# Optimization experiments

Measured on AMD Instinct MI355X. Metric: run time of the kernel, lower is better.

The kernel has to match this reference:

```python
import jax
import jax.numpy as jnp
from jax import lax
import numpy as np

V, E, H, H2, C, B, L = 50000, 256, 256, 128, 12, 64, 512
START, STOP = 10, 11
IMPOSSIBLE = -10000.0


def setup_inputs() -> dict:
    key = jax.random.key(0)
    ks = jax.random.split(key, 30)
    rn = lambda k, s, sc=0.1: jax.random.normal(k, s, jnp.float32) * sc
    d = {}
    d["sentence"] = jax.random.randint(ks[0], (B, L), 0, V)
    d["masks"] = jnp.ones((B, L), jnp.float32)
    d["emb_table"] = rn(ks[1], (V, E))
    i = 2
    for layer, din in ((1, E), (2, H)):
        for dr in ("f", "r"):
            d["w_ih_%s%d" % (dr, layer)] = rn(ks[i], (4 * H2, din)); i += 1
            d["w_hh_%s%d" % (dr, layer)] = rn(ks[i], (4 * H2, H2)); i += 1
            d["b_ih_%s%d" % (dr, layer)] = rn(ks[i], (4 * H2,)); i += 1
            d["b_hh_%s%d" % (dr, layer)] = rn(ks[i], (4 * H2,)); i += 1
    d["w_out"] = rn(ks[i], (C, H)); i += 1
    d["b_out"] = rn(ks[i], (C,)); i += 1
    tr = jax.random.normal(ks[i], (C, C), jnp.float32); i += 1
    d["transitions"] = tr.at[START, :].set(IMPOSSIBLE).at[:, STOP].set(IMPOSSIBLE)
    for nm in ("h0_1", "c0_1", "h0_2", "c0_2"):
        d[nm] = rn(ks[i], (2, B, H2), 1.0); i += 1
    return d


def _lstm_dir(x, h0, c0, w_ih, w_hh, b_ih, b_hh, reverse):
    # x: [L, B, Din]; PyTorch LSTM gate order: i, f, g, o
    b = b_ih + b_hh
    def step(carry, xt):
        h, c = carry
        g = xt @ w_ih.T + h @ w_hh.T + b  # [B, 4*H2]
        i, f, gg, o = jnp.split(g, 4, axis=-1)
        c = jax.nn.sigmoid(f) * c + jax.nn.sigmoid(i) * jnp.tanh(gg)
        h = jax.nn.sigmoid(o) * jnp.tanh(c)
        return (h, c), h
    _, hs = lax.scan(step, (h0, c0), x, reverse=reverse)
    return hs  # [L, B, H2]


def _bilstm(x, h0, c0, pf, pr):
    hf = _lstm_dir(x, h0[0], c0[0], *pf, reverse=False)
    hr = _lstm_dir(x, h0[1], c0[1], *pr, reverse=True)
    return jnp.concatenate([hf, hr], axis=-1)  # [L, B, H]


def reference(sentence, masks, emb_table,
              w_ih_f1, w_hh_f1, b_ih_f1, b_hh_f1, w_ih_r1, w_hh_r1, b_ih_r1, b_hh_r1,
              w_ih_f2, w_hh_f2, b_ih_f2, b_hh_f2, w_ih_r2, w_hh_r2, b_ih_r2, b_hh_r2,
              w_out, b_out, transitions, h0_1, c0_1, h0_2, c0_2):
    Bb, Ll = sentence.shape
    # faithful to the original: embedding output is .view()'d (reshaped), not transposed
    embeds = emb_table[sentence].reshape(Ll, Bb, -1)  # [L, B, E]
    out1 = _bilstm(embeds, h0_1, c0_1,
                   (w_ih_f1, w_hh_f1, b_ih_f1, b_hh_f1),
                   (w_ih_r1, w_hh_r1, b_ih_r1, b_hh_r1))
    out2 = _bilstm(out1, h0_2, c0_2,
                   (w_ih_f2, w_hh_f2, b_ih_f2, b_hh_f2),
                   (w_ih_r2, w_hh_r2, b_ih_r2, b_hh_r2))
    feats = out2.reshape(Bb, Ll, -1) @ w_out.T + b_out  # [B, L, C]
    Cc = feats.shape[-1]

    # Viterbi forward pass over time
    init = jnp.full((Bb, Cc), IMPOSSIBLE, jnp.float32).at[:, START].set(0.0)
    def vstep(ms, inp):
        emit, m = inp  # [B, C], [B]
        acc = ms[:, None, :] + transitions[None]  # [B, C_to, C_from]
        bp = jnp.argmax(acc, axis=-1)             # [B, C]
        sc = jnp.max(acc, axis=-1) + emit
        mm = m[:, None]
        return sc * mm + ms * (1.0 - mm), bp
    final, bps = lax.scan(vstep, init, (feats.transpose(1, 0, 2), masks.T))  # bps: [L, B, C]
    final = final + transitions[STOP]
    best_score = final.max(axis=-1)        # [B]
    best_tag = jnp.argmax(final, axis=-1)  # [B]

    # vectorized backtrace: tag[len-1] = best_tag; tag[t] = bps[t+1][tag[t+1]]
    lengths = masks.sum(axis=1).astype(jnp.int32)  # [B]
    bps_next = jnp.concatenate([bps[1:], bps[-1:]], axis=0)  # bps_next[t] = bps[t+1]
    ts = jnp.arange(Ll)
    def bstep(cur, inp):
        t, bpn = inp  # bpn: [B, C]
        nxt = jnp.take_along_axis(bpn, cur[:, None], axis=1)[:, 0]
        new = jnp.where(t >= lengths - 1, best_tag, nxt)
        return new, new
    _, path = lax.scan(bstep, best_tag, (ts, bps_next), reverse=True)  # [L, B]
    path = path.T  # [B, L]
    path = jnp.where(ts[None, :] < lengths[:, None], path, 0)
    return best_score, path
```

## Files before the change

kernel.cpp:

```cpp
#include <hip/hip_runtime.h>
#include <math.h>

#define VSZ   50000
#define EDIM  256
#define HDIM  256
#define H2D   128
#define NCLS  12
#define NB    64
#define NL    512
#define G4    512
#define NNC   1024
#define MM    32768
#define START_TAG 10
#define STOP_TAG  11
#define IMPOSSIBLE -10000.0f

__device__ __forceinline__ float sigmoidf_(float x) {
    return 1.0f / (1.0f + expf(-x));
}

template <bool GATHER>
__global__ __launch_bounds__(256)
void gemm_gates(const float* __restrict__ A,
                const int*   __restrict__ gidx,
                const float* __restrict__ wf,
                const float* __restrict__ wr,
                const float* __restrict__ bihf, const float* __restrict__ bhhf,
                const float* __restrict__ bihr, const float* __restrict__ bhhr,
                float* __restrict__ out)
{
    __shared__ __align__(16) float As[32][132];
    __shared__ __align__(16) float Bs[32][132];

    const int tid = threadIdx.x;
    const int n0  = blockIdx.x * 128;
    const int m0  = blockIdx.y * 128;

    const int w    = tid >> 6;
    const int lane = tid & 63;
    const int wm   = w >> 1;
    const int wn   = w & 1;
    const int am   = lane >> 3;
    const int bn   = lane & 7;
    const int ma   = wm * 64 + am * 8;
    const int nb   = wn * 64 + bn * 8;

    float acc[8][8];
#pragma unroll
    for (int i = 0; i < 8; ++i)
#pragma unroll
        for (int jj = 0; jj < 8; ++jj) acc[i][jj] = 0.0f;

    const bool   fwdside = (n0 < 512);
    const float* wsrc    = fwdside ? wf : wr;
    const int    nbase   = fwdside ? n0 : (n0 - 512);

    int srcA[4];
#pragma unroll
    for (int it = 0; it < 4; ++it) {
        int li  = tid + it * 256;
        int row = m0 + (li >> 3);
        srcA[it] = GATHER ? gidx[row] : row;
    }

    for (int kt = 0; kt < 8; ++kt) {
#pragma unroll
        for (int it = 0; it < 4; ++it) {
            int li = tid + it * 256;
            int r  = li >> 3;
            int c4 = li & 7;
            float4 v = ((const float4*)A)[(size_t)srcA[it] * 64 + kt * 8 + c4];
            As[c4 * 4 + 0][r] = v.x;
            As[c4 * 4 + 1][r] = v.y;
            As[c4 * 4 + 2][r] = v.z;
            As[c4 * 4 + 3][r] = v.w;
        }
#pragma unroll
        for (int it = 0; it < 4; ++it) {
            int li = tid + it * 256;
            int r  = li >> 3;
            int c4 = li & 7;
            float4 v = ((const float4*)wsrc)[(size_t)(nbase + r) * 64 + kt * 8 + c4];
            Bs[c4 * 4 + 0][r] = v.x;
            Bs[c4 * 4 + 1][r] = v.y;
            Bs[c4 * 4 + 2][r] = v.z;
            Bs[c4 * 4 + 3][r] = v.w;
        }
        __syncthreads();

#pragma unroll
        for (int k = 0; k < 32; ++k) {
            float a[8], b[8];
            *(float4*)&a[0] = *(const float4*)&As[k][ma];
            *(float4*)&a[4] = *(const float4*)&As[k][ma + 4];
            *(float4*)&b[0] = *(const float4*)&Bs[k][nb];
            *(float4*)&b[4] = *(const float4*)&Bs[k][nb + 4];
#pragma unroll
            for (int i = 0; i < 8; ++i)
#pragma unroll
                for (int jj = 0; jj < 8; ++jj)
                    acc[i][jj] = fmaf(a[i], b[jj], acc[i][jj]);
        }
        __syncthreads();
    }

    float bias[8];
#pragma unroll
    for (int jj = 0; jj < 8; ++jj) {
        int gn = n0 + nb + jj;
        bias[jj] = fwdside ? (bihf[gn] + bhhf[gn]) : (bihr[gn - 512] + bhhr[gn - 512]);
    }
#pragma unroll
    for (int i = 0; i < 8; ++i) {
        int m = m0 + ma + i;
        float4 s0, s1;
        s0.x = acc[i][0] + bias[0]; s0.y = acc[i][1] + bias[1];
        s0.z = acc[i][2] + bias[2]; s0.w = acc[i][3] + bias[3];
        s1.x = acc[i][4] + bias[4]; s1.y = acc[i][5] + bias[5];
        s1.z = acc[i][6] + bias[6]; s1.w = acc[i][7] + bias[7];
        float4* op = (float4*)(out + (size_t)m * NNC + n0 + nb);
        op[0] = s0;
        op[1] = s1;
    }
}

__global__ __launch_bounds__(512, 2)
void lstm_rec(const float* __restrict__ gx,
              const float* __restrict__ whf,
              const float* __restrict__ whr,
              const float* __restrict__ h0,
              const float* __restrict__ c0,
              float* __restrict__ out)
{
    __shared__ __align__(16) float h_lds[H2D];
    __shared__ __align__(16) float gates[G4];

    const int j   = threadIdx.x;
    const int dir = blockIdx.x >> 6;
    const int bb  = blockIdx.x & 63;
    const float* W = dir ? whr : whf;

    float4 w4[32];
#pragma unroll
    for (int k = 0; k < 32; ++k)
        w4[k] = ((const float4*)W)[(size_t)j * 32 + k];
#pragma unroll
    for (int k = 0; k < 32; ++k)
        asm volatile("" : "+v"(w4[k].x), "+v"(w4[k].y), "+v"(w4[k].z), "+v"(w4[k].w));

    float creg = 0.0f;
    if (j < H2D) {
        h_lds[j] = h0[dir * (NB * H2D) + bb * H2D + j];
        creg     = c0[dir * (NB * H2D) + bb * H2D + j];
    }
    __syncthreads();

    const float4* h4 = (const float4*)h_lds;
    const int chunk = j >> 7;
    const size_t gx_off = (size_t)dir * 512 + j;

    const int tfirst = dir ? (NL - 1) : 0;
    float gx_cur = gx[((size_t)tfirst * NB + bb) * NNC + gx_off];

    for (int ti = 0; ti < NL; ++ti) {
        const int t = dir ? (NL - 1 - ti) : ti;
        const size_t m = (size_t)t * NB + bb;

        float d0 = 0.f, d1 = 0.f, d2 = 0.f, d3 = 0.f;
#pragma unroll
        for (int k = 0; k < 32; ++k) {
            const float4 hv = h4[k];
            d0 = fmaf(w4[k].x, hv.x, d0);
            d1 = fmaf(w4[k].y, hv.y, d1);
            d2 = fmaf(w4[k].z, hv.z, d2);
            d3 = fmaf(w4[k].w, hv.w, d3);
        }
        const float pre = ((d0 + d1) + (d2 + d3)) + gx_cur;
        const float act = (chunk == 2) ? tanhf(pre) : sigmoidf_(pre);
        gates[j] = act;
        __syncthreads();

        if (ti + 1 < NL) {
            const int tn = dir ? (NL - 2 - ti) : (ti + 1);
            gx_cur = gx[((size_t)tn * NB + bb) * NNC + gx_off];
        }

        if (j < H2D) {
            const float ig = gates[j];
            const float fg = gates[j + 128];
            const float gg = gates[j + 256];
            const float og = gates[j + 384];
            creg = fg * creg + ig * gg;
            const float hnew = og * tanhf(creg);
            h_lds[j] = hnew;
            out[m * HDIM + dir * H2D + j] = hnew;
        }
        __syncthreads();
    }
}

__global__ __launch_bounds__(256)
void feats_kernel(const float* __restrict__ out2,
                  const float* __restrict__ w_out,
                  const float* __restrict__ b_out,
                  float* __restrict__ feats)
{
    __shared__ __align__(16) float wl[NCLS * HDIM];
    const int tid = threadIdx.x;
#pragma unroll
    for (int i = 0; i < NCLS; ++i) wl[tid + i * 256] = w_out[tid + i * 256];
    __syncthreads();

    const int m = blockIdx.x * 256 + tid;
    float acc[NCLS];
#pragma unroll
    for (int c = 0; c < NCLS; ++c) acc[c] = 0.0f;

    const float4* x4 = (const float4*)out2 + (size_t)m * 64;
    const float4* w4 = (const float4*)wl;
    for (int k4 = 0; k4 < 64; ++k4) {
        float4 x = x4[k4];
#pragma unroll
        for (int c = 0; c < NCLS; ++c) {
            float4 wv = w4[c * 64 + k4];
            acc[c] = fmaf(x.x, wv.x, acc[c]);
            acc[c] = fmaf(x.y, wv.y, acc[c]);
            acc[c] = fmaf(x.z, wv.z, acc[c]);
            acc[c] = fmaf(x.w, wv.w, acc[c]);
        }
    }
#pragma unroll
    for (int c = 0; c < NCLS; ++c)
        feats[(size_t)m * NCLS + c] = acc[c] + b_out[c];
}

__global__ __launch_bounds__(64)
void viterbi_crf(const float* __restrict__ feats,
                 const float* __restrict__ masks,
                 const float* __restrict__ trans,
                 float* __restrict__ out)
{
    __shared__ unsigned char bpl[NL][NCLS];
    __shared__ float pathl[NL];

    const int b    = blockIdx.x;
    const int lane = threadIdx.x;

    float tr[NCLS];
#pragma unroll
    for (int jj = 0; jj < NCLS; ++jj)
        tr[jj] = (lane < NCLS) ? trans[lane * NCLS + jj] : 0.0f;

    float msv = (lane == START_TAG) ? 0.0f : IMPOSSIBLE;
    float len = 0.0f;

    float emit_n = (lane < NCLS) ? feats[((size_t)b * NL) * NCLS + lane] : 0.0f;
    float mt_n   = masks[b * NL];

    for (int t = 0; t < NL; ++t) {
        const float emit = emit_n;
        const float mt   = mt_n;
        if (t + 1 < NL) {
            emit_n = (lane < NCLS) ? feats[((size_t)b * NL + t + 1) * NCLS + lane] : 0.0f;
            mt_n   = masks[b * NL + t + 1];
        }
        len += mt;

        float best = -3.4e38f;
        int   bj   = 0;
#pragma unroll
        for (int jj = 0; jj < NCLS; ++jj) {
            float msj = __shfl(msv, jj);
            float v   = msj + tr[jj];
            if (v > best) { best = v; bj = jj; }
        }
        const float sc = best + emit;
        msv = mt * sc + (1.0f - mt) * msv;
        if (lane < NCLS)
            bpl[t][lane] = (unsigned char)bj;
    }

    const float fin = (lane < NCLS) ? (msv + trans[STOP_TAG * NCLS + lane]) : -3.4e38f;
    float bv = -3.4e38f;
    int   bt = 0;
#pragma unroll
    for (int jj = 0; jj < NCLS; ++jj) {
        float v = __shfl(fin, jj);
        if (v > bv) { bv = v; bt = jj; }
    }
    if (lane == 0) out[b] = bv;

    const int ilen = (int)(len + 0.5f);

    __syncthreads();

    int cur = bt;
    for (int t = NL - 1; t >= 0; --t) {
        const int tb  = (t == NL - 1) ? (NL - 1) : (t + 1);
        const int nxt = bpl[tb][cur];
        const int val = (t >= ilen - 1) ? bt : nxt;
        cur = val;
        if (lane == 0) pathl[t] = (t < ilen) ? (float)val : 0.0f;
    }
    __syncthreads();

    float* po = out + 64 + (size_t)b * NL;
#pragma unroll
    for (int i = 0; i < NL / 64; ++i)
        po[lane + i * 64] = pathl[lane + i * 64];
}

extern "C" void kernel_launch(void* const* d_in, const int* in_sizes, int n_in,
                              void* d_out, int out_size, void* d_ws, size_t ws_size,
                              hipStream_t stream)
{
    const int*   sentence = (const int*)  d_in[0];
    const float* masks    = (const float*)d_in[1];
    const float* emb      = (const float*)d_in[2];
    const float* w_ih_f1  = (const float*)d_in[3];
    const float* w_hh_f1  = (const float*)d_in[4];
    const float* b_ih_f1  = (const float*)d_in[5];
    const float* b_hh_f1  = (const float*)d_in[6];
    const float* w_ih_r1  = (const float*)d_in[7];
    const float* w_hh_r1  = (const float*)d_in[8];
    const float* b_ih_r1  = (const float*)d_in[9];
    const float* b_hh_r1  = (const float*)d_in[10];
    const float* w_ih_f2  = (const float*)d_in[11];
    const float* w_hh_f2  = (const float*)d_in[12];
    const float* b_ih_f2  = (const float*)d_in[13];
    const float* b_hh_f2  = (const float*)d_in[14];
    const float* w_ih_r2  = (const float*)d_in[15];
    const float* w_hh_r2  = (const float*)d_in[16];
    const float* b_ih_r2  = (const float*)d_in[17];
    const float* b_hh_r2  = (const float*)d_in[18];
    const float* w_out    = (const float*)d_in[19];
    const float* b_out    = (const float*)d_in[20];
    const float* trans    = (const float*)d_in[21];
    const float* h0_1     = (const float*)d_in[22];
    const float* c0_1     = (const float*)d_in[23];
    const float* h0_2     = (const float*)d_in[24];
    const float* c0_2     = (const float*)d_in[25];

    float* gx    = (float*)d_ws;
    float* out1  = gx   + (size_t)MM * NNC;
    float* out2  = out1 + (size_t)MM * HDIM;
    float* feats = out2 + (size_t)MM * HDIM;

    dim3 gemm_grid(NNC / 128, MM / 128);

    gemm_gates<true><<<gemm_grid, 256, 0, stream>>>(
        emb, sentence, w_ih_f1, w_ih_r1, b_ih_f1, b_hh_f1, b_ih_r1, b_hh_r1, gx);
    lstm_rec<<<128, 512, 0, stream>>>(gx, w_hh_f1, w_hh_r1, h0_1, c0_1, out1);

    gemm_gates<false><<<gemm_grid, 256, 0, stream>>>(
        out1, nullptr, w_ih_f2, w_ih_r2, b_ih_f2, b_hh_f2, b_ih_r2, b_hh_r2, gx);
    lstm_rec<<<128, 512, 0, stream>>>(gx, w_hh_f2, w_hh_r2, h0_2, c0_2, out2);

    feats_kernel<<<MM / 256, 256, 0, stream>>>(out2, w_out, b_out, feats);
    viterbi_crf<<<NB, 64, 0, stream>>>(feats, masks, trans, (float*)d_out);
}
```

Baseline: 1.872 ms.

## Split LSTM recurrence K-dimension across 1024 threads with readlane broadcast

The recurrent kernel now launches 1024 threads per block, and each thread holds half a weight row (64 values) in registers. The hidden state is broadcast within each wavefront via readlane instead of LDS float4 reads. Partial dot products are summed through shared memory, and the 128 update threads apply all four gate activations and prefetch their own gx values. The goal is to shorten the serial per-timestep latency, at the cost of more threads, more scalar readlane work and higher register pressure per step.

```diff
diff --git a/kernel.cpp b/kernel.cpp
--- a/kernel.cpp
+++ b/kernel.cpp
@@ -124,7 +124,7 @@
     }
 }
 
-__global__ __launch_bounds__(512, 2)
+__global__ __launch_bounds__(1024, 4)
 void lstm_rec(const float* __restrict__ gx,
               const float* __restrict__ whf,
               const float* __restrict__ whr,
@@ -133,67 +133,91 @@
               float* __restrict__ out)
 {
     __shared__ __align__(16) float h_lds[H2D];
-    __shared__ __align__(16) float gates[G4];
-
-    const int j   = threadIdx.x;
+    __shared__ __align__(16) float partial[1024];
+
+    const int tid = threadIdx.x;
+    const int row = tid & 511;
+    const int kh  = tid >> 9;
     const int dir = blockIdx.x >> 6;
     const int bb  = blockIdx.x & 63;
     const float* W = dir ? whr : whf;
 
-    float4 w4[32];
-#pragma unroll
-    for (int k = 0; k < 32; ++k)
-        w4[k] = ((const float4*)W)[(size_t)j * 32 + k];
-#pragma unroll
-    for (int k = 0; k < 32; ++k)
-        asm volatile("" : "+v"(w4[k].x), "+v"(w4[k].y), "+v"(w4[k].z), "+v"(w4[k].w));
+    float wreg[64];
+    {
+        const float4* wp = (const float4*)(W + (size_t)row * H2D + kh * 64);
+#pragma unroll
+        for (int k = 0; k < 16; ++k) {
+            float4 v = wp[k];
+            wreg[4 * k + 0] = v.x; wreg[4 * k + 1] = v.y;
+            wreg[4 * k + 2] = v.z; wreg[4 * k + 3] = v.w;
+        }
+    }
 
     float creg = 0.0f;
-    if (j < H2D) {
-        h_lds[j] = h0[dir * (NB * H2D) + bb * H2D + j];
-        creg     = c0[dir * (NB * H2D) + bb * H2D + j];
+    if (tid < H2D) {
+        h_lds[tid] = h0[dir * (NB * H2D) + bb * H2D + tid];
+        creg       = c0[dir * (NB * H2D) + bb * H2D + tid];
     }
     __syncthreads();
 
-    const float4* h4 = (const float4*)h_lds;
-    const int chunk = j >> 7;
-    const size_t gx_off = (size_t)dir * 512 + j;
-
-    const int tfirst = dir ? (NL - 1) : 0;
-    float gx_cur = gx[((size_t)tfirst * NB + bb) * NNC + gx_off];
+    const int  lane = tid & 63;
+    const bool upd  = (tid < H2D);
+
+    const size_t gxbase = (size_t)dir * 512 + tid;
+    float gxc[4] = {0.f, 0.f, 0.f, 0.f};
+    if (upd) {
+        const int tf = dir ? (NL - 1) : 0;
+        const size_t mo = ((size_t)tf * NB + bb) * NNC + gxbase;
+#pragma unroll
+        for (int k = 0; k < 4; ++k) gxc[k] = gx[mo + 128 * k];
+    }
 
     for (int ti = 0; ti < NL; ++ti) {
         const int t = dir ? (NL - 1 - ti) : ti;
         const size_t m = (size_t)t * NB + bb;
 
-        float d0 = 0.f, d1 = 0.f, d2 = 0.f, d3 = 0.f;
-#pragma unroll
-        for (int k = 0; k < 32; ++k) {
-            const float4 hv = h4[k];
-            d0 = fmaf(w4[k].x, hv.x, d0);
-            d1 = fmaf(w4[k].y, hv.y, d1);
-            d2 = fmaf(w4[k].z, hv.z, d2);
-            d3 = fmaf(w4[k].w, hv.w, d3);
-        }
-        const float pre = ((d0 + d1) + (d2 + d3)) + gx_cur;
-        const float act = (chunk == 2) ? tanhf(pre) : sigmoidf_(pre);
-        gates[j] = act;
+        const float hv  = h_lds[kh * 64 + lane];
+        const int   hvi = __float_as_int(hv);
+
+        float gxn[4];
+        if (upd && ti + 1 < NL) {
+            const int tn = dir ? (NL - 2 - ti) : (ti + 1);
+            const size_t mo = ((size_t)tn * NB + bb) * NNC + gxbase;
+#pragma unroll
+            for (int k = 0; k < 4; ++k) gxn[k] = gx[mo + 128 * k];
+        }
+
+        float a0 = 0.f, a1 = 0.f, a2 = 0.f, a3 = 0.f;
+#pragma unroll
+        for (int i = 0; i < 64; i += 4) {
+            const float s0 = __int_as_float(__builtin_amdgcn_readlane(hvi, i + 0));
+            const float s1 = __int_as_float(__builtin_amdgcn_readlane(hvi, i + 1));
+            const float s2 = __int_as_float(__builtin_amdgcn_readlane(hvi, i + 2));
+            const float s3 = __int_as_float(__builtin_amdgcn_readlane(hvi, i + 3));
+            a0 = fmaf(wreg[i + 0], s0, a0);
+            a1 = fmaf(wreg[i + 1], s1, a1);
+            a2 = fmaf(wreg[i + 2], s2, a2);
+            a3 = fmaf(wreg[i + 3], s3, a3);
+        }
+        const float half = (a0 + a1) + (a2 + a3);
+        partial[tid] = half;
         __syncthreads();
 
-        if (ti + 1 < NL) {
-            const int tn = dir ? (NL - 2 - ti) : (ti + 1);
-            gx_cur = gx[((size_t)tn * NB + bb) * NNC + gx_off];
-        }
-
-        if (j < H2D) {
-            const float ig = gates[j];
-            const float fg = gates[j + 128];
-            const float gg = gates[j + 256];
-            const float og = gates[j + 384];
+        if (upd) {
+            const float pi = (half + partial[tid + 512]) + gxc[0];
+            const float pf = (partial[tid + 128] + partial[tid + 640]) + gxc[1];
+            const float pg = (partial[tid + 256] + partial[tid + 768]) + gxc[2];
+            const float po = (partial[tid + 384] + partial[tid + 896]) + gxc[3];
+            const float ig = sigmoidf_(pi);
+            const float fg = sigmoidf_(pf);
+            const float gg = tanhf(pg);
+            const float og = sigmoidf_(po);
             creg = fg * creg + ig * gg;
             const float hnew = og * tanhf(creg);
-            h_lds[j] = hnew;
-            out[m * HDIM + dir * H2D + j] = hnew;
+            h_lds[tid] = hnew;
+            out[m * HDIM + dir * H2D + tid] = hnew;
+#pragma unroll
+            for (int k = 0; k < 4; ++k) gxc[k] = gxn[k];
         }
         __syncthreads();
     }
@@ -350,11 +374,11 @@
 
     gemm_gates<true><<<gemm_grid, 256, 0, stream>>>(
         emb, sentence, w_ih_f1, w_ih_r1, b_ih_f1, b_hh_f1, b_ih_r1, b_hh_r1, gx);
-    lstm_rec<<<128, 512, 0, stream>>>(gx, w_hh_f1, w_hh_r1, h0_1, c0_1, out1);
+    lstm_rec<<<128, 1024, 0, stream>>>(gx, w_hh_f1, w_hh_r1, h0_1, c0_1, out1);
 
     gemm_gates<false><<<gemm_grid, 256, 0, stream>>>(
         out1, nullptr, w_ih_f2, w_ih_r2, b_ih_f2, b_hh_f2, b_ih_r2, b_hh_r2, gx);
-    lstm_rec<<<128, 512, 0, stream>>>(gx, w_hh_f2, w_hh_r2, h0_2, c0_2, out2);
+    lstm_rec<<<128, 1024, 0, stream>>>(gx, w_hh_f2, w_hh_r2, h0_2, c0_2, out2);
 
     feats_kernel<<<MM / 256, 256, 0, stream>>>(out2, w_out, b_out, feats);
     viterbi_crf<<<NB, 64, 0, stream>>>(feats, masks, trans, (float*)d_out);
```

After: 2.229 ms. 19.1% more time.
